# Optimization experiments

Measured on AMD Instinct MI355X. Metric: run time of the kernel, lower is better.

Reference implementation:

```python
import jax, jax.numpy as jnp
import numpy as np

N_ITER = 2          # GenSP n_iter
M_COEF = 0.0        # GenSP M (grid strength)
AFF_SOFTMAX = 1.0   # GenSP affinity_softmax
NEG_INF = -1e30


def setup_inputs() -> dict:
    key = jax.random.key(0)
    x = jax.random.normal(key, (4, 64, 256, 256), dtype=jnp.float32)
    return {"x": x, "stoken": 16}


def _candidates(H, W, sh, sw, nH, nW):
    # 3x3 neighborhood of each pixel's initial superpixel (SSN / get_abs_indices)
    bi = jnp.arange(H) // sh
    bj = jnp.arange(W) // sw
    di = jnp.repeat(jnp.array([-1, 0, 1]), 3)   # (9,)
    dj = jnp.tile(jnp.array([-1, 0, 1]), 3)     # (9,)
    ci = bi[:, None, None] + di                 # (H,1,9)
    cj = bj[None, :, None] + dj                 # (1,W,9)
    valid = (ci >= 0) & (ci < nH) & (cj >= 0) & (cj < nW)        # (H,W,9)
    cand = jnp.clip(ci, 0, nH - 1) * nW + jnp.clip(cj, 0, nW - 1)  # (H,W,9)
    cand = jnp.broadcast_to(cand, (H, W, 9)).reshape(H * W, 9)
    valid = jnp.broadcast_to(valid, (H, W, 9)).reshape(H * W, 9)
    return cand, valid


def _affinity(feats, cent, cand, valid, nS):
    # feats: (B,Cf,P)  cent: (B,Cf,nS)  cand/valid: (P,9)
    B, Cf, P = feats.shape
    dot = jnp.einsum('bcp,bcs->bps', feats, cent)            # (B,P,nS) GEMM
    f2 = jnp.sum(feats * feats, axis=1)                      # (B,P)
    c2 = jnp.sum(cent * cent, axis=1)                        # (B,nS)
    dot9 = jnp.take_along_axis(dot, cand[None], axis=2)      # (B,P,9)
    dist = f2[..., None] + c2[:, cand] - 2.0 * dot9          # l2 distance (B,P,9)
    logits = jnp.where(valid[None], -AFF_SOFTMAX * dist, NEG_INF)
    aff9 = jax.nn.softmax(logits, axis=-1)                   # softmax_order 'v0'
    aff9 = jnp.where(valid[None], aff9, 0.0)
    # dense scatter: A[b, cand[p,k], p] += aff9[b,p,k]  -> (B,nS,P)
    pidx = jnp.arange(P)[:, None]
    A = jnp.zeros((B, nS, P), feats.dtype).at[:, cand, pidx].add(aff9)
    return A


def reference(x, stoken):
    B, C, H, W = x.shape
    sh = sw = int(stoken)
    nH, nW = (H - 1) // sh + 1, (W - 1) // sw + 1
    nS, P = nH * nW, H * W
    # append_grid: concat scaled pixel-coordinate channels (M / stoken)
    gi, gj = jnp.meshgrid(jnp.arange(H, dtype=x.dtype), jnp.arange(W, dtype=x.dtype), indexing='ij')
    grid = jnp.broadcast_to((M_COEF / sh) * jnp.stack([gi, gj]), (B, 2, H, W))
    feats = jnp.concatenate([x, grid], axis=1)               # (B,C+2,H,W)
    Cf = C + 2
    # init centroids: adaptive_avg_pool2d == block mean (H,W divisible by stoken)
    cent = feats.reshape(B, Cf, nH, sh, nW, sw).mean(axis=(3, 5)).reshape(B, Cf, nS)
    feats = feats.reshape(B, Cf, P)
    cand, valid = _candidates(H, W, sh, sw, nH, nW)
    A = None
    for k in range(N_ITER):
        A = _affinity(feats, cent, cand, valid, nS)          # (B,nS,P)
        if k < N_ITER - 1:
            num = jnp.einsum('bsp,bcp->bcs', A, feats)       # (B,Cf,nS)
            den = jnp.sum(A, axis=2)[:, None, :] + 1e-16
            cent = num / den
    return A
```

## Files before the change

kernel.cpp:

```cpp
#include <hip/hip_runtime.h>


#define PP 65536

typedef __attribute__((ext_vector_type(8))) short short8;
typedef __attribute__((ext_vector_type(4))) float f32x4;

__device__ __forceinline__ unsigned short f2bf(float f) {
  unsigned u = __float_as_uint(f);
  u += 0x7fff + ((u >> 16) & 1);
  return (unsigned short)(u >> 16);
}

__global__ __launch_bounds__(256) void k_init(const float* __restrict__ x,
                                              float* __restrict__ cent0,
                                              float4* __restrict__ zero4) {
  __shared__ float blk[64];
  int t = threadIdx.x;
  int wg = blockIdx.x;
  int cg = wg & 15, bi = (wg >> 4) & 15, b = wg >> 8;
  int tid = wg * 256 + t;
  if (tid < 16640) zero4[tid] = make_float4(0.f, 0.f, 0.f, 0.f);
  if (t < 64) blk[t] = 0.f;
  __syncthreads();
  int sub = t >> 6, j4 = t & 63;
#pragma unroll
  for (int q = 0; q < 4; q++) {
    int c = cg * 4 + q;
    const float4* xp4 =
        (const float4*)(x + ((long)(b * 64 + c) << 16) + ((bi * 16 + sub * 4) << 8)) + j4;
    float4 a = make_float4(0.f, 0.f, 0.f, 0.f);
#pragma unroll
    for (int r = 0; r < 4; r++) {
      float4 v = xp4[r * 64];
      a.x += v.x; a.y += v.y; a.z += v.z; a.w += v.w;
    }
    float ps = a.x + a.y + a.z + a.w;
    ps += __shfl_xor(ps, 1);
    ps += __shfl_xor(ps, 2);
    if ((j4 & 3) == 0) atomicAdd(&blk[(j4 >> 2) * 4 + q], ps);
  }
  __syncthreads();
  if (t < 64) {
    int sj = t >> 2, q = t & 3;
    cent0[(((b << 8) + bi * 16 + sj) << 6) + cg * 4 + q] = blk[t] * (1.f / 256.f);
  }
}

__global__ __launch_bounds__(256) void k_stat(const float* __restrict__ x,
                                              const float* __restrict__ cent,
                                              float* __restrict__ num,
                                              float* __restrict__ den) {
  __shared__ __align__(16) unsigned short xbf[64 * 264];
  __shared__ __align__(16) unsigned short affbf[16 * 264];
  __shared__ float cent_s[9 * 64];
  __shared__ float c2p[72];
  __shared__ float c2_s[9];
  __shared__ float den_s[36];
  __shared__ int scand[9];

  int t = threadIdx.x;
  int wg = blockIdx.x;
  int bj = wg & 15, bi = (wg >> 4) & 15, b = wg >> 8;

  if (t < 9) {
    int di = t / 3 - 1, dj = t % 3 - 1;
    int ci = bi + di, cj = bj + dj;
    int sc = min(max(ci, 0), 15) * 16 + min(max(cj, 0), 15);
    bool valid = ((unsigned)ci < 16u) && ((unsigned)cj < 16u);
    scand[t] = valid ? sc : (-1 - sc);
  }
  for (int o = t; o < 144; o += 256) {
    int k = o >> 4, f4 = o & 15;
    int di = k / 3 - 1, dj = k % 3 - 1;
    int sc = min(max(bi + di, 0), 15) * 16 + min(max(bj + dj, 0), 15);
    *(float4*)&cent_s[k * 64 + f4 * 4] =
        *(const float4*)(cent + (((b << 8) + sc) << 6) + f4 * 4);
  }
  __syncthreads();
  if (t < 72) {
    int k = t >> 3, pt = t & 7;
    float s = 0.f;
#pragma unroll
    for (int m = 0; m < 8; m++) { float v = cent_s[k * 64 + pt * 8 + m]; s += v * v; }
    c2p[t] = s;
  }
  __syncthreads();
  if (t < 9) {
    float s = 0.f;
#pragma unroll
    for (int m = 0; m < 8; m++) s += c2p[t * 8 + m];
    c2_s[t] = s;
  }
  __syncthreads();

  int vbits = 0;
#pragma unroll
  for (int k = 0; k < 9; k++) {
    int ci = bi + k / 3 - 1, cj = bj + k % 3 - 1;
    if ((unsigned)ci < 16u && (unsigned)cj < 16u) vbits |= 1 << k;
  }

  int r = t >> 4, col = t & 15;
  const float* base = x + ((long)(b * 64) << 16) + ((bi * 16 + r) << 8) + (bj * 16 + col);
  float acc[9];
#pragma unroll
  for (int k = 0; k < 9; k++) acc[k] = 0.f;
#pragma unroll 8
  for (int c = 0; c < 64; c++) {
    float xv = base[(long)c << 16];
    xbf[c * 264 + t] = f2bf(xv);
#pragma unroll
    for (int k = 0; k < 9; k++) acc[k] = fmaf(xv, cent_s[k * 64 + c], acc[k]);
  }
  float mx = -1e30f;
#pragma unroll
  for (int k = 0; k < 9; k++) {
    float l = 2.f * acc[k] - c2_s[k];
    acc[k] = ((vbits >> k) & 1) ? l : -1e30f;
    mx = fmaxf(mx, acc[k]);
  }
  float sum = 0.f;
#pragma unroll
  for (int k = 0; k < 9; k++) {
    acc[k] = __expf(acc[k] - mx);
    sum += acc[k];
  }
  float rs = 1.f / sum;
#pragma unroll
  for (int k = 0; k < 9; k++) {
    acc[k] *= rs;
    affbf[k * 264 + t] = f2bf(acc[k]);
  }

  int lane = t & 63, w = t >> 6;
#pragma unroll
  for (int k = 0; k < 9; k++) {
    float v = acc[k];
    v += __shfl_xor(v, 1);
    v += __shfl_xor(v, 2);
    v += __shfl_xor(v, 4);
    v += __shfl_xor(v, 8);
    v += __shfl_xor(v, 16);
    v += __shfl_xor(v, 32);
    if (lane == 0) den_s[w * 9 + k] = v;
  }
  __syncthreads();
  if (t < 9) {
    float d = den_s[t] + den_s[9 + t] + den_s[18 + t] + den_s[27 + t];
    int sc = scand[t]; sc = sc >= 0 ? sc : (-1 - sc);
    atomicAdd(&den[(b << 8) + sc], d);
  }

  int mrow = lane & 15;
  int quad = lane >> 4;
  f32x4 dacc = {0.f, 0.f, 0.f, 0.f};
#pragma unroll
  for (int ks = 0; ks < 8; ks++) {
    int p0 = ks * 32 + quad * 8;
    short8 a = *(const short8*)&xbf[(w * 16 + mrow) * 264 + p0];
    short8 bf = *(const short8*)&affbf[mrow * 264 + p0];
    dacc = __builtin_amdgcn_mfma_f32_16x16x32_bf16(a, bf, dacc, 0, 0, 0);
  }
  int kcol = lane & 15;
  if (kcol < 9) {
    int sc = scand[kcol]; sc = sc >= 0 ? sc : (-1 - sc);
    float* np = num + (((b << 8) + sc) << 6) + w * 16 + quad * 4;
    atomicAdd(&np[0], dacc[0]);
    atomicAdd(&np[1], dacc[1]);
    atomicAdd(&np[2], dacc[2]);
    atomicAdd(&np[3], dacc[3]);
  }
}

__global__ __launch_bounds__(256) void k_out(const float* __restrict__ x,
                                             const float* __restrict__ num,
                                             const float* __restrict__ den,
                                             f32x4* __restrict__ out4) {
  __shared__ float cent_s[48 * 68];
  __shared__ float den_s[48];
  __shared__ float c2p[384];
  __shared__ float c2_s[48];
  __shared__ float aff_t[9 * 260];

  int t = threadIdx.x;
  int wg = blockIdx.x;
  int h = wg & 1, i = (wg >> 1) & 255, b = wg >> 9;
  int bi = i >> 4;

  if (t < 48) {
    int ci = min(max(bi - 1 + (t >> 4), 0), 15);
    int cj = t & 15;
    den_s[t] = den[(b << 8) + ci * 16 + cj] + 1e-16f;
  }
  __syncthreads();
  for (int o = t; o < 768; o += 256) {
    int lr = o >> 4, f4i = o & 15;
    int ci = min(max(bi - 1 + (lr >> 4), 0), 15);
    int cj = lr & 15;
    float4 v = *(const float4*)(num + (((b << 8) + ci * 16 + cj) << 6) + f4i * 4);
    float inv = 1.f / den_s[lr];
    v.x *= inv; v.y *= inv; v.z *= inv; v.w *= inv;
    *(float4*)&cent_s[lr * 68 + f4i * 4] = v;
  }
  __syncthreads();
  for (int o = t; o < 384; o += 256) {
    int lr = o >> 3, pt = o & 7;
    float s = 0.f;
#pragma unroll
    for (int m = 0; m < 8; m++) { float v = cent_s[lr * 68 + pt * 8 + m]; s += v * v; }
    c2p[o] = s;
  }
  __syncthreads();
  if (t < 48) {
    float s = 0.f;
#pragma unroll
    for (int m = 0; m < 8; m++) s += c2p[t * 8 + m];
    c2_s[t] = s;
  }
  __syncthreads();

  int j = t, bj = j >> 4;
  int cidx[9];
  float c2k[9];
  int vbits = 0;
#pragma unroll
  for (int k = 0; k < 9; k++) {
    int di = k / 3 - 1, dj = k % 3 - 1;
    int ciu = bi + di, cju = bj + dj;
    if ((unsigned)ciu < 16u && (unsigned)cju < 16u) vbits |= 1 << k;
    int lidx = (di + 1) * 16 + min(max(cju, 0), 15);
    cidx[k] = lidx * 68;
    c2k[k] = c2_s[lidx];
  }
  const float* base = x + ((long)(b * 64) << 16) + (i << 8) + j;
  float acc[9];
#pragma unroll
  for (int k = 0; k < 9; k++) acc[k] = 0.f;
#pragma unroll 8
  for (int c = 0; c < 64; c++) {
    float xv = base[(long)c << 16];
#pragma unroll
    for (int k = 0; k < 9; k++) acc[k] = fmaf(xv, cent_s[cidx[k] + c], acc[k]);
  }
  float mx = -1e30f;
#pragma unroll
  for (int k = 0; k < 9; k++) {
    float l = 2.f * acc[k] - c2k[k];
    acc[k] = ((vbits >> k) & 1) ? l : -1e30f;
    mx = fmaxf(mx, acc[k]);
  }
  float sum = 0.f;
#pragma unroll
  for (int k = 0; k < 9; k++) {
    acc[k] = __expf(acc[k] - mx);
    sum += acc[k];
  }
  float rs = 1.f / sum;
#pragma unroll
  for (int k = 0; k < 9; k++) aff_t[k * 260 + j] = acc[k] * rs;
  __syncthreads();

  f32x4* obase = out4 + ((long)(b << 8) << 14) + (i << 6) + (t & 63);
  int j4 = t & 63;
  int w = t >> 6;
  int s0 = h << 7;
#pragma unroll 4
  for (int m = 0; m < 32; m++) {
    int s = s0 | (m << 2) | w;
    f32x4 v = {0.f, 0.f, 0.f, 0.f};
    int di = (s >> 4) - bi;
    if ((unsigned)(di + 1) <= 2u) {
      int dj = (s & 15) - (j4 >> 2);
      if ((unsigned)(dj + 1) <= 2u) {
        int k = (di + 1) * 3 + dj + 1;
        v = *(const f32x4*)&aff_t[k * 260 + (j4 << 2)];
      }
    }
    __builtin_nontemporal_store(v, &obase[(long)s << 14]);
  }
}

extern "C" void kernel_launch(void* const* d_in, const int* in_sizes, int n_in,
                              void* d_out, int out_size, void* d_ws, size_t ws_size,
                              hipStream_t stream) {
  const float* x = (const float*)d_in[0];
  float* out = (float*)d_out;
  float* ws = (float*)d_ws;

  float* num   = ws;
  float* den   = ws + 65536;
  float* cent0 = ws + 66560;

  k_init<<<1024, 256, 0, stream>>>(x, cent0, (float4*)ws);
  k_stat<<<1024, 256, 0, stream>>>(x, cent0, num, den);
  k_out<<<2048, 256, 0, stream>>>(x, num, den, (f32x4*)out);
}
```

Measured before the change: 353.0 us.

## Zero output in init kernel and write only nonzero affinity entries

The dense output is now zeroed by 1024 extra workgroups added to the init kernel, which runs concurrently with the centroid pooling. The final kernel then writes only the 9-neighbour nonzero entries for each row strip instead of streaming the full (nS,P) block including zeros, and uses half as many workgroups. This moves the bulk zero fill off the critical compute kernel and drops the per-element branch logic. In exchange the output now gets a scattered second write pass that is no longer nontemporal.

```diff
diff --git a/kernel.cpp b/kernel.cpp
--- a/kernel.cpp
+++ b/kernel.cpp
@@ -1,7 +1,5 @@
 #include <hip/hip_runtime.h>
 
-
-#define PP 65536
 
 typedef __attribute__((ext_vector_type(8))) short short8;
 typedef __attribute__((ext_vector_type(4))) float f32x4;
@@ -12,12 +10,23 @@
   return (unsigned short)(u >> 16);
 }
 
-__global__ __launch_bounds__(256) void k_init(const float* __restrict__ x,
-                                              float* __restrict__ cent0,
-                                              float4* __restrict__ zero4) {
+__global__ __launch_bounds__(256) void k_init2(const float* __restrict__ x,
+                                               float* __restrict__ cent0,
+                                               float4* __restrict__ zero4,
+                                               f32x4* __restrict__ out4) {
   __shared__ float blk[64];
   int t = threadIdx.x;
   int wg = blockIdx.x;
+
+  if (wg >= 1024) {
+    int q = wg - 1024;
+    f32x4* op = out4 + ((long)q << 14);
+    const f32x4 z = {0.f, 0.f, 0.f, 0.f};
+#pragma unroll 8
+    for (int m = 0; m < 64; m++) op[m * 256 + t] = z;
+    return;
+  }
+
   int cg = wg & 15, bi = (wg >> 4) & 15, b = wg >> 8;
   int tid = wg * 256 + t;
   if (tid < 16640) zero4[tid] = make_float4(0.f, 0.f, 0.f, 0.f);
@@ -173,19 +182,19 @@
   }
 }
 
-__global__ __launch_bounds__(256) void k_out(const float* __restrict__ x,
-                                             const float* __restrict__ num,
-                                             const float* __restrict__ den,
-                                             f32x4* __restrict__ out4) {
-  __shared__ float cent_s[48 * 68];
+__global__ __launch_bounds__(256) void k_strip(const float* __restrict__ x,
+                                               const float* __restrict__ num,
+                                               const float* __restrict__ den,
+                                               f32x4* __restrict__ out4) {
+  __shared__ __align__(16) float cent_s[48 * 68];
+  __shared__ __align__(16) float aff_t[9 * 260];
+  __shared__ float c2p[384];
   __shared__ float den_s[48];
-  __shared__ float c2p[384];
   __shared__ float c2_s[48];
-  __shared__ float aff_t[9 * 260];
 
   int t = threadIdx.x;
   int wg = blockIdx.x;
-  int h = wg & 1, i = (wg >> 1) & 255, b = wg >> 9;
+  int i = wg & 255, b = wg >> 8;
   int bi = i >> 4;
 
   if (t < 48) {
@@ -261,23 +270,23 @@
   for (int k = 0; k < 9; k++) aff_t[k * 260 + j] = acc[k] * rs;
   __syncthreads();
 
-  f32x4* obase = out4 + ((long)(b << 8) << 14) + (i << 6) + (t & 63);
-  int j4 = t & 63;
-  int w = t >> 6;
-  int s0 = h << 7;
-#pragma unroll 4
-  for (int m = 0; m < 32; m++) {
-    int s = s0 | (m << 2) | w;
-    f32x4 v = {0.f, 0.f, 0.f, 0.f};
-    int di = (s >> 4) - bi;
-    if ((unsigned)(di + 1) <= 2u) {
-      int dj = (s & 15) - (j4 >> 2);
-      if ((unsigned)(dj + 1) <= 2u) {
-        int k = (di + 1) * 3 + dj + 1;
-        v = *(const f32x4*)&aff_t[k * 260 + (j4 << 2)];
-      }
+  long obase = ((long)(b << 8)) << 14;
+#pragma unroll
+  for (int step = 0; step < 3; step++) {
+    int o = step * 256 + t;
+    if (o >= 576) break;
+    int si_idx = o / 192;
+    int rem = o - si_idx * 192;
+    int sj = rem / 12;
+    int u4 = rem - sj * 12;
+    int si = bi - 1 + si_idx;
+    int j4 = 4 * sj - 4 + u4;
+    if ((unsigned)si < 16u && (unsigned)j4 < 64u) {
+      int k = si_idx * 3 + (sj - (j4 >> 2)) + 1;
+      f32x4 v = *(const f32x4*)&aff_t[k * 260 + (j4 << 2)];
+      int s = si * 16 + sj;
+      out4[obase + ((long)s << 14) + (i << 6) + j4] = v;
     }
-    __builtin_nontemporal_store(v, &obase[(long)s << 14]);
   }
 }
 
@@ -292,7 +301,7 @@
   float* den   = ws + 65536;
   float* cent0 = ws + 66560;
 
-  k_init<<<1024, 256, 0, stream>>>(x, cent0, (float4*)ws);
+  k_init2<<<2048, 256, 0, stream>>>(x, cent0, (float4*)ws, (f32x4*)out);
   k_stat<<<1024, 256, 0, stream>>>(x, cent0, num, den);
-  k_out<<<2048, 256, 0, stream>>>(x, num, den, (f32x4*)out);
-}
+  k_strip<<<1024, 256, 0, stream>>>(x, num, den, (f32x4*)out);
+}
```

Result: slower. 366.0 us (+3.7%).
